# Kernel tuning notes

Measured on AMD Instinct MI355X. Metric: run time of the kernel, lower is better.

The kernel has to match this reference:

```python
import jax, jax.numpy as jnp
import numpy as np

B, R, NT = 1, 384, 4        # batch, num_res, num_templates
C_IN = 128                   # rep_2d num_c (pair channels)
C_KV = 64                    # template pair channels
H, C = 4, 64                 # num_heads, attention_num_c


def setup_inputs() -> dict:
    key = jax.random.key(0)
    ks = jax.random.split(key, 7)
    s = lambda fan_in: 1.0 / np.sqrt(fan_in)
    return {
        "z2d": jax.random.normal(ks[0], (B, R, R, C_IN), jnp.float32),
        "t2d": jax.random.normal(ks[1], (B, NT, R, R, C_KV), jnp.float32),
        # weights stored [in, out] (torch nn.Linear applies x @ W.T)
        "Wq": jax.random.normal(ks[2], (C_IN, H * C), jnp.float32) * s(C_IN),
        "Wk": jax.random.normal(ks[3], (C_KV, H * C), jnp.float32) * s(C_KV),
        "Wv": jax.random.normal(ks[4], (C_KV, H * C), jnp.float32) * s(C_KV),
        "Wo": jax.random.normal(ks[5], (H * C, C_IN), jnp.float32) * s(H * C),
        "bo": jax.random.normal(ks[6], (C_IN,), jnp.float32) * s(H * C),
    }


def reference(z2d, t2d, Wq, Wk, Wv, Wo, bo):
    b, r, _, c_in = z2d.shape
    nt = t2d.shape[1]
    P = r * r  # flattened residue-pair axis

    z = z2d.reshape(b, P, 1, c_in)                             # [b, P, 1, c_in]
    t = jnp.transpose(t2d, (0, 2, 3, 1, 4)).reshape(b, P, nt, -1)  # [b, P, K, c_kv]

    q = (z @ Wq).reshape(b, P, 1, H, C) * C ** (-0.5)          # [b, P, 1, h, c]
    k = (t @ Wk).reshape(b, P, nt, H, C)                       # [b, P, k, h, c]
    v = (t @ Wv).reshape(b, P, nt, H, C)

    logits = jnp.einsum('bpqhc,bpkhc->bphqk', q, k)            # softmax over k templates
    weights = jax.nn.softmax(logits, axis=-1)
    weighted_avg = jnp.einsum('bphqk,bpkhc->bpqhc', weights, v)  # [b, P, 1, h, c]

    out = weighted_avg.reshape(b, P, 1, H * C) @ Wo + bo
    return out.reshape(b, r, r, c_in)
```

## Files before the change

kernel.cpp:

```cpp
#include <hip/hip_runtime.h>
#include <hip/hip_bf16.h>

#define R_   384
#define P_   (R_ * R_)
#define NT_  4
#define CIN  128
#define CKV  64
#define NH   4
#define HC   256

#define TP   64
#define LDZ  136
#define LDA  280

typedef __attribute__((ext_vector_type(8))) short bf16x8;
typedef __attribute__((ext_vector_type(4))) float f32x4;
typedef __attribute__((ext_vector_type(4))) uint  u32x4;
typedef __attribute__((ext_vector_type(2))) __bf16 bfv2;

#if defined(__has_builtin)
#if __has_builtin(__builtin_amdgcn_fdot2_f32_bf16)
#define HAS_DOT2BF 1
#endif
#endif

__device__ __forceinline__ ushort f2bf_s(float f) {
    uint32_t u = __float_as_uint(f);
    u += 0x7FFFu + ((u >> 16) & 1u);
    return (ushort)(u >> 16);
}
__device__ __forceinline__ uint packbf2(float lo, float hi) {
    return (uint)f2bf_s(lo) | ((uint)f2bf_s(hi) << 16);
}
__device__ __forceinline__ uint2 pack4(const float4 v) {
    uint2 r; r.x = packbf2(v.x, v.y); r.y = packbf2(v.z, v.w); return r;
}
__device__ __forceinline__ float bflo(uint t) { return __uint_as_float(t << 16); }
__device__ __forceinline__ float bfhi(uint t) { return __uint_as_float(t & 0xffff0000u); }

__device__ __forceinline__ float dot2bf(uint a, uint b, float acc) {
#ifdef HAS_DOT2BF
    union { uint u; bfv2 v; } ua, ub;
    ua.u = a; ub.u = b;
    return __builtin_amdgcn_fdot2_f32_bf16(ua.v, ub.v, acc, false);
#else
    float r = fmaf(bflo(a), bflo(b), acc);
    return fmaf(bfhi(a), bfhi(b), r);
#endif
}

__global__ __launch_bounds__(256) void precompute_mg(
        const float* __restrict__ Wq, const float* __restrict__ Wk,
        const float* __restrict__ Wv, const float* __restrict__ Wo,
        ushort* __restrict__ Mt, ushort* __restrict__ Gt) {
    int tid = blockIdx.x * blockDim.x + threadIdx.x;
    if (tid < HC * CIN) {
        int n = tid >> 7, ci = tid & 127;
        int h = n >> 6, j = n & 63;
        float acc = 0.f;
        for (int c = 0; c < 64; ++c)
            acc += Wq[ci * HC + h * 64 + c] * Wk[j * HC + h * 64 + c];
        Mt[n * CIN + ci] = f2bf_s(acc * 0.125f);
    } else {
        int t = tid - HC * CIN;
        int co = t >> 8, n = t & 255;
        int h = n >> 6, j = n & 63;
        float acc = 0.f;
        for (int c = 0; c < 64; ++c)
            acc += Wv[j * HC + h * 64 + c] * Wo[(h * 64 + c) * CIN + co];
        Gt[co * HC + n] = f2bf_s(acc);
    }
}

__global__ __launch_bounds__(256, 2) void tpa_fused(
        const float* __restrict__ z2d, const float* __restrict__ t2d,
        const ushort* __restrict__ Mt, const ushort* __restrict__ Gt,
        const float* __restrict__ bo, float* __restrict__ out) {

    __shared__ ushort s0[TP * LDA];
    __shared__ ushort sT[TP * LDA];

    const int tid  = threadIdx.x;
    const int lane = tid & 63;
    const int wv   = tid >> 6;
    const int lr   = lane & 15;
    const int lk   = (lane >> 4) << 3;
    const int pg0  = blockIdx.x * TP;

    bf16x8 B1[4][4];
    #pragma unroll
    for (int kt = 0; kt < 4; ++kt)
        #pragma unroll
        for (int nt = 0; nt < 4; ++nt)
            B1[kt][nt] = *(const bf16x8*)(Mt + (wv * 64 + nt * 16 + lr) * CIN + kt * 32 + lk);
    bf16x8 B2[8][2];
    #pragma unroll
    for (int kt = 0; kt < 8; ++kt)
        #pragma unroll
        for (int nt = 0; nt < 2; ++nt)
            B2[kt][nt] = *(const bf16x8*)(Gt + (wv * 32 + nt * 16 + lr) * HC + kt * 32 + lk);

    const float bias0 = bo[wv * 32 + lr];
    const float bias1 = bo[wv * 32 + 16 + lr];

    #pragma unroll
    for (int i = 0; i < 8; ++i) {
        int idx = (i * 256 + tid) * 4, p = idx >> 7, c = idx & 127;
        float4 v = *(const float4*)(z2d + (size_t)(pg0 + p) * CIN + c);
        *(uint2*)&s0[p * LDZ + c] = pack4(v);
    }
    #pragma unroll
    for (int k = 0; k < NT_; ++k) {
        const float* src = t2d + ((size_t)k * P_ + pg0) * CKV;
        #pragma unroll
        for (int i = 0; i < 4; ++i) {
            int idx = (i * 256 + tid) * 4, p = idx >> 6, c = idx & 63;
            float4 v = *(const float4*)(src + p * 64 + c);
            *(uint2*)&sT[p * LDA + k * 64 + c] = pack4(v);
        }
    }
    __syncthreads();

    f32x4 acc1[4][4];
    #pragma unroll
    for (int mt = 0; mt < 4; ++mt)
        #pragma unroll
        for (int nt = 0; nt < 4; ++nt)
            acc1[mt][nt] = (f32x4){0.f, 0.f, 0.f, 0.f};
    #pragma unroll
    for (int kt = 0; kt < 4; ++kt) {
        bf16x8 af[4];
        #pragma unroll
        for (int mt = 0; mt < 4; ++mt)
            af[mt] = *(const bf16x8*)&s0[(mt * 16 + lr) * LDZ + kt * 32 + lk];
        #pragma unroll
        for (int mt = 0; mt < 4; ++mt)
            #pragma unroll
            for (int nt = 0; nt < 4; ++nt)
                acc1[mt][nt] = __builtin_amdgcn_mfma_f32_16x16x32_bf16(
                    af[mt], B1[kt][nt], acc1[mt][nt], 0, 0, 0);
    }
    __syncthreads();

    #pragma unroll
    for (int mt = 0; mt < 4; ++mt) {
        int row = mt * 16 + ((lane >> 4) << 2);
        #pragma unroll
        for (int nt = 0; nt < 4; ++nt) {
            int n = wv * 64 + nt * 16 + lr;
            #pragma unroll
            for (int r = 0; r < 4; ++r)
                s0[(row + r) * LDA + n] = f2bf_s(acc1[mt][nt][r]);
        }
    }
    asm volatile("s_waitcnt lgkmcnt(0)" ::: "memory");
    __builtin_amdgcn_sched_barrier(0);

    {
        ushort* arow = &s0[lane * LDA + wv * 64];
        const ushort* trow = &sT[lane * LDA];

        u32x4 a4[8];
        #pragma unroll
        for (int q = 0; q < 8; ++q) a4[q] = *(const u32x4*)&arow[q * 8];

        float lg[4];
        #pragma unroll
        for (int k = 0; k < 4; ++k) {
            float s = 0.f;
            #pragma unroll
            for (int q = 0; q < 8; ++q) {
                u32x4 tq = *(const u32x4*)&trow[k * 64 + q * 8];
                #pragma unroll
                for (int e = 0; e < 4; ++e)
                    s = dot2bf(a4[q][e], tq[e], s);
            }
            lg[k] = s;
        }
        float mx = fmaxf(fmaxf(lg[0], lg[1]), fmaxf(lg[2], lg[3]));
        float w0 = __expf(lg[0] - mx), w1 = __expf(lg[1] - mx);
        float w2 = __expf(lg[2] - mx), w3 = __expf(lg[3] - mx);
        float inv = 1.f / (w0 + w1 + w2 + w3);
        w0 *= inv; w1 *= inv; w2 *= inv; w3 *= inv;

        #pragma unroll
        for (int q = 0; q < 8; ++q) {
            u32x4 t0 = *(const u32x4*)&trow[q * 8];
            u32x4 t1 = *(const u32x4*)&trow[64 + q * 8];
            u32x4 t2 = *(const u32x4*)&trow[128 + q * 8];
            u32x4 t3 = *(const u32x4*)&trow[192 + q * 8];
            u32x4 o;
            #pragma unroll
            for (int e = 0; e < 4; ++e) {
                float lo = w0 * bflo(t0[e]) + w1 * bflo(t1[e]) + w2 * bflo(t2[e]) + w3 * bflo(t3[e]);
                float hi = w0 * bfhi(t0[e]) + w1 * bfhi(t1[e]) + w2 * bfhi(t2[e]) + w3 * bfhi(t3[e]);
                o[e] = packbf2(lo, hi);
            }
            *(u32x4*)&arow[q * 8] = o;
        }
    }
    __syncthreads();

    f32x4 acc2[4][2];
    #pragma unroll
    for (int mt = 0; mt < 4; ++mt)
        #pragma unroll
        for (int nt = 0; nt < 2; ++nt)
            acc2[mt][nt] = (f32x4){0.f, 0.f, 0.f, 0.f};
    #pragma unroll
    for (int kt = 0; kt < 8; ++kt) {
        bf16x8 af[4];
        #pragma unroll
        for (int mt = 0; mt < 4; ++mt)
            af[mt] = *(const bf16x8*)&s0[(mt * 16 + lr) * LDA + kt * 32 + lk];
        #pragma unroll
        for (int mt = 0; mt < 4; ++mt)
            #pragma unroll
            for (int nt = 0; nt < 2; ++nt)
                acc2[mt][nt] = __builtin_amdgcn_mfma_f32_16x16x32_bf16(
                    af[mt], B2[kt][nt], acc2[mt][nt], 0, 0, 0);
    }

    #pragma unroll
    for (int nt = 0; nt < 2; ++nt) {
        int co = wv * 32 + nt * 16 + lr;
        float bias = nt ? bias1 : bias0;
        #pragma unroll
        for (int mt = 0; mt < 4; ++mt) {
            int row = mt * 16 + ((lane >> 4) << 2);
            #pragma unroll
            for (int r = 0; r < 4; ++r)
                out[(size_t)(pg0 + row + r) * CIN + co] = acc2[mt][nt][r] + bias;
        }
    }
}

extern "C" void kernel_launch(void* const* d_in, const int* in_sizes, int n_in,
                              void* d_out, int out_size, void* d_ws, size_t ws_size,
                              hipStream_t stream) {
    const float* z2d = (const float*)d_in[0];
    const float* t2d = (const float*)d_in[1];
    const float* Wq  = (const float*)d_in[2];
    const float* Wk  = (const float*)d_in[3];
    const float* Wv  = (const float*)d_in[4];
    const float* Wo  = (const float*)d_in[5];
    const float* bo  = (const float*)d_in[6];

    ushort* Mt = (ushort*)d_ws;
    ushort* Gt = Mt + HC * CIN;

    precompute_mg<<<(2 * HC * CIN) / 256, 256, 0, stream>>>(Wq, Wk, Wv, Wo, Mt, Gt);
    tpa_fused<<<P_ / TP, 256, 0, stream>>>(z2d, t2d, Mt, Gt, bo, (float*)d_out);
}
```

Baseline: 82.40 us.

## Stream z and templates directly from global, drop template LDS staging, swap MFMA operands

The z tile is now loaded straight from global memory into MFMA fragments instead of being staged through LDS. Template rows are read directly from global in fp32 for both the logit and weighted-sum passes. This removes the sT buffer and halves shared memory, and the occupancy hint rises from 2 to 3 blocks. MFMA operands are swapped so outputs come out transposed, which allows packed 8-byte LDS writes and float4 global stores. In exchange each thread reads every template row from global twice, and the logits now use fp32 template values rather than bf16.

```diff
diff --git a/kernel.cpp b/kernel.cpp
--- a/kernel.cpp
+++ b/kernel.cpp
@@ -1,5 +1,4 @@
 #include <hip/hip_runtime.h>
-#include <hip/hip_bf16.h>
 
 #define R_   384
 #define P_   (R_ * R_)
@@ -10,19 +9,11 @@
 #define HC   256
 
 #define TP   64
-#define LDZ  136
 #define LDA  280
 
 typedef __attribute__((ext_vector_type(8))) short bf16x8;
 typedef __attribute__((ext_vector_type(4))) float f32x4;
 typedef __attribute__((ext_vector_type(4))) uint  u32x4;
-typedef __attribute__((ext_vector_type(2))) __bf16 bfv2;
-
-#if defined(__has_builtin)
-#if __has_builtin(__builtin_amdgcn_fdot2_f32_bf16)
-#define HAS_DOT2BF 1
-#endif
-#endif
 
 __device__ __forceinline__ ushort f2bf_s(float f) {
     uint32_t u = __float_as_uint(f);
@@ -32,22 +23,10 @@
 __device__ __forceinline__ uint packbf2(float lo, float hi) {
     return (uint)f2bf_s(lo) | ((uint)f2bf_s(hi) << 16);
 }
-__device__ __forceinline__ uint2 pack4(const float4 v) {
-    uint2 r; r.x = packbf2(v.x, v.y); r.y = packbf2(v.z, v.w); return r;
-}
 __device__ __forceinline__ float bflo(uint t) { return __uint_as_float(t << 16); }
 __device__ __forceinline__ float bfhi(uint t) { return __uint_as_float(t & 0xffff0000u); }
 
-__device__ __forceinline__ float dot2bf(uint a, uint b, float acc) {
-#ifdef HAS_DOT2BF
-    union { uint u; bfv2 v; } ua, ub;
-    ua.u = a; ub.u = b;
-    return __builtin_amdgcn_fdot2_f32_bf16(ua.v, ub.v, acc, false);
-#else
-    float r = fmaf(bflo(a), bflo(b), acc);
-    return fmaf(bfhi(a), bfhi(b), r);
-#endif
-}
+union BF8 { bf16x8 v; uint u[4]; };
 
 __global__ __launch_bounds__(256) void precompute_mg(
         const float* __restrict__ Wq, const float* __restrict__ Wk,
@@ -72,19 +51,19 @@
     }
 }
 
-__global__ __launch_bounds__(256, 2) void tpa_fused(
+__global__ __launch_bounds__(256, 3) void tpa_fused(
         const float* __restrict__ z2d, const float* __restrict__ t2d,
         const ushort* __restrict__ Mt, const ushort* __restrict__ Gt,
         const float* __restrict__ bo, float* __restrict__ out) {
 
-    __shared__ ushort s0[TP * LDA];
-    __shared__ ushort sT[TP * LDA];
+    __shared__ ushort sA[TP * LDA];
 
     const int tid  = threadIdx.x;
     const int lane = tid & 63;
     const int wv   = tid >> 6;
     const int lr   = lane & 15;
-    const int lk   = (lane >> 4) << 3;
+    const int g    = lane >> 4;
+    const int g8   = g << 3;
     const int pg0  = blockIdx.x * TP;
 
     bf16x8 B1[4][4];
@@ -92,145 +71,157 @@
     for (int kt = 0; kt < 4; ++kt)
         #pragma unroll
         for (int nt = 0; nt < 4; ++nt)
-            B1[kt][nt] = *(const bf16x8*)(Mt + (wv * 64 + nt * 16 + lr) * CIN + kt * 32 + lk);
+            B1[kt][nt] = *(const bf16x8*)(Mt + (wv * 64 + nt * 16 + lr) * CIN + kt * 32 + g8);
+
+    f32x4 acc1[4][4];
+    #pragma unroll
+    for (int nt = 0; nt < 4; ++nt)
+        #pragma unroll
+        for (int mt = 0; mt < 4; ++mt)
+            acc1[nt][mt] = (f32x4){0.f, 0.f, 0.f, 0.f};
+
+    #pragma unroll
+    for (int kt = 0; kt < 4; ++kt) {
+        bf16x8 zf[4];
+        #pragma unroll
+        for (int mt = 0; mt < 4; ++mt) {
+            const float* zp = z2d + (size_t)(pg0 + mt * 16 + lr) * CIN + kt * 32 + g8;
+            float4 z0 = *(const float4*)zp;
+            float4 z1 = *(const float4*)(zp + 4);
+            BF8 zb;
+            zb.u[0] = packbf2(z0.x, z0.y); zb.u[1] = packbf2(z0.z, z0.w);
+            zb.u[2] = packbf2(z1.x, z1.y); zb.u[3] = packbf2(z1.z, z1.w);
+            zf[mt] = zb.v;
+        }
+        #pragma unroll
+        for (int nt = 0; nt < 4; ++nt)
+            #pragma unroll
+            for (int mt = 0; mt < 4; ++mt)
+                acc1[nt][mt] = __builtin_amdgcn_mfma_f32_16x16x32_bf16(
+                    B1[kt][nt], zf[mt], acc1[nt][mt], 0, 0, 0);
+    }
+
+    #pragma unroll
+    for (int nt = 0; nt < 4; ++nt) {
+        int n0 = wv * 64 + nt * 16 + g * 4;
+        #pragma unroll
+        for (int mt = 0; mt < 4; ++mt) {
+            int p = mt * 16 + lr;
+            uint2 w;
+            w.x = packbf2(acc1[nt][mt][0], acc1[nt][mt][1]);
+            w.y = packbf2(acc1[nt][mt][2], acc1[nt][mt][3]);
+            *(uint2*)&sA[p * LDA + n0] = w;
+        }
+    }
+
     bf16x8 B2[8][2];
     #pragma unroll
     for (int kt = 0; kt < 8; ++kt)
         #pragma unroll
         for (int nt = 0; nt < 2; ++nt)
-            B2[kt][nt] = *(const bf16x8*)(Gt + (wv * 32 + nt * 16 + lr) * HC + kt * 32 + lk);
-
-    const float bias0 = bo[wv * 32 + lr];
-    const float bias1 = bo[wv * 32 + 16 + lr];
-
-    #pragma unroll
-    for (int i = 0; i < 8; ++i) {
-        int idx = (i * 256 + tid) * 4, p = idx >> 7, c = idx & 127;
-        float4 v = *(const float4*)(z2d + (size_t)(pg0 + p) * CIN + c);
-        *(uint2*)&s0[p * LDZ + c] = pack4(v);
-    }
-    #pragma unroll
-    for (int k = 0; k < NT_; ++k) {
-        const float* src = t2d + ((size_t)k * P_ + pg0) * CKV;
-        #pragma unroll
-        for (int i = 0; i < 4; ++i) {
-            int idx = (i * 256 + tid) * 4, p = idx >> 6, c = idx & 63;
-            float4 v = *(const float4*)(src + p * 64 + c);
-            *(uint2*)&sT[p * LDA + k * 64 + c] = pack4(v);
-        }
-    }
+            B2[kt][nt] = *(const bf16x8*)(Gt + (wv * 32 + nt * 16 + lr) * HC + kt * 32 + g8);
+    float4 b4[2];
+    #pragma unroll
+    for (int nt = 0; nt < 2; ++nt)
+        b4[nt] = *(const float4*)(bo + wv * 32 + nt * 16 + g * 4);
+
     __syncthreads();
 
-    f32x4 acc1[4][4];
-    #pragma unroll
-    for (int mt = 0; mt < 4; ++mt)
-        #pragma unroll
-        for (int nt = 0; nt < 4; ++nt)
-            acc1[mt][nt] = (f32x4){0.f, 0.f, 0.f, 0.f};
-    #pragma unroll
-    for (int kt = 0; kt < 4; ++kt) {
-        bf16x8 af[4];
-        #pragma unroll
-        for (int mt = 0; mt < 4; ++mt)
-            af[mt] = *(const bf16x8*)&s0[(mt * 16 + lr) * LDZ + kt * 32 + lk];
-        #pragma unroll
-        for (int mt = 0; mt < 4; ++mt)
-            #pragma unroll
-            for (int nt = 0; nt < 4; ++nt)
-                acc1[mt][nt] = __builtin_amdgcn_mfma_f32_16x16x32_bf16(
-                    af[mt], B1[kt][nt], acc1[mt][nt], 0, 0, 0);
-    }
-    __syncthreads();
-
-    #pragma unroll
-    for (int mt = 0; mt < 4; ++mt) {
-        int row = mt * 16 + ((lane >> 4) << 2);
-        #pragma unroll
-        for (int nt = 0; nt < 4; ++nt) {
-            int n = wv * 64 + nt * 16 + lr;
-            #pragma unroll
-            for (int r = 0; r < 4; ++r)
-                s0[(row + r) * LDA + n] = f2bf_s(acc1[mt][nt][r]);
-        }
-    }
-    asm volatile("s_waitcnt lgkmcnt(0)" ::: "memory");
-    __builtin_amdgcn_sched_barrier(0);
-
     {
-        ushort* arow = &s0[lane * LDA + wv * 64];
-        const ushort* trow = &sT[lane * LDA];
+        const int h = g;
+        const int p = wv * 16 + lr;
+        const ushort* arow = &sA[p * LDA + h * 64];
 
         u32x4 a4[8];
         #pragma unroll
         for (int q = 0; q < 8; ++q) a4[q] = *(const u32x4*)&arow[q * 8];
 
-        float lg[4];
-        #pragma unroll
-        for (int k = 0; k < 4; ++k) {
-            float s = 0.f;
-            #pragma unroll
-            for (int q = 0; q < 8; ++q) {
-                u32x4 tq = *(const u32x4*)&trow[k * 64 + q * 8];
-                #pragma unroll
-                for (int e = 0; e < 4; ++e)
-                    s = dot2bf(a4[q][e], tq[e], s);
-            }
-            lg[k] = s;
-        }
-        float mx = fmaxf(fmaxf(lg[0], lg[1]), fmaxf(lg[2], lg[3]));
-        float w0 = __expf(lg[0] - mx), w1 = __expf(lg[1] - mx);
-        float w2 = __expf(lg[2] - mx), w3 = __expf(lg[3] - mx);
+        const float* tk0 = t2d + ((size_t)0 * P_ + pg0 + p) * CKV;
+        const float* tk1 = t2d + ((size_t)1 * P_ + pg0 + p) * CKV;
+        const float* tk2 = t2d + ((size_t)2 * P_ + pg0 + p) * CKV;
+        const float* tk3 = t2d + ((size_t)3 * P_ + pg0 + p) * CKV;
+
+        float lg0 = 0.f, lg1 = 0.f, lg2 = 0.f, lg3 = 0.f;
+        #pragma unroll
+        for (int q4 = 0; q4 < 16; ++q4) {
+            float4 t0 = *(const float4*)(tk0 + q4 * 4);
+            float4 t1 = *(const float4*)(tk1 + q4 * 4);
+            float4 t2 = *(const float4*)(tk2 + q4 * 4);
+            float4 t3 = *(const float4*)(tk3 + q4 * 4);
+            uint ua = a4[q4 >> 1][(q4 & 1) * 2 + 0];
+            uint ub = a4[q4 >> 1][(q4 & 1) * 2 + 1];
+            float a0 = bflo(ua), a1 = bfhi(ua), a2 = bflo(ub), a3 = bfhi(ub);
+            lg0 = fmaf(a0, t0.x, lg0); lg0 = fmaf(a1, t0.y, lg0);
+            lg0 = fmaf(a2, t0.z, lg0); lg0 = fmaf(a3, t0.w, lg0);
+            lg1 = fmaf(a0, t1.x, lg1); lg1 = fmaf(a1, t1.y, lg1);
+            lg1 = fmaf(a2, t1.z, lg1); lg1 = fmaf(a3, t1.w, lg1);
+            lg2 = fmaf(a0, t2.x, lg2); lg2 = fmaf(a1, t2.y, lg2);
+            lg2 = fmaf(a2, t2.z, lg2); lg2 = fmaf(a3, t2.w, lg2);
+            lg3 = fmaf(a0, t3.x, lg3); lg3 = fmaf(a1, t3.y, lg3);
+            lg3 = fmaf(a2, t3.z, lg3); lg3 = fmaf(a3, t3.w, lg3);
+        }
+        float mx = fmaxf(fmaxf(lg0, lg1), fmaxf(lg2, lg3));
+        float w0 = __expf(lg0 - mx), w1 = __expf(lg1 - mx);
+        float w2 = __expf(lg2 - mx), w3 = __expf(lg3 - mx);
         float inv = 1.f / (w0 + w1 + w2 + w3);
         w0 *= inv; w1 *= inv; w2 *= inv; w3 *= inv;
 
-        #pragma unroll
-        for (int q = 0; q < 8; ++q) {
-            u32x4 t0 = *(const u32x4*)&trow[q * 8];
-            u32x4 t1 = *(const u32x4*)&trow[64 + q * 8];
-            u32x4 t2 = *(const u32x4*)&trow[128 + q * 8];
-            u32x4 t3 = *(const u32x4*)&trow[192 + q * 8];
+        ushort* urow = &sA[p * LDA + h * 64];
+        #pragma unroll
+        for (int q8 = 0; q8 < 8; ++q8) {
+            float4 t0a = *(const float4*)(tk0 + q8 * 8), t0b = *(const float4*)(tk0 + q8 * 8 + 4);
+            float4 t1a = *(const float4*)(tk1 + q8 * 8), t1b = *(const float4*)(tk1 + q8 * 8 + 4);
+            float4 t2a = *(const float4*)(tk2 + q8 * 8), t2b = *(const float4*)(tk2 + q8 * 8 + 4);
+            float4 t3a = *(const float4*)(tk3 + q8 * 8), t3b = *(const float4*)(tk3 + q8 * 8 + 4);
+            float u0 = w0*t0a.x + w1*t1a.x + w2*t2a.x + w3*t3a.x;
+            float u1 = w0*t0a.y + w1*t1a.y + w2*t2a.y + w3*t3a.y;
+            float u2 = w0*t0a.z + w1*t1a.z + w2*t2a.z + w3*t3a.z;
+            float u3 = w0*t0a.w + w1*t1a.w + w2*t2a.w + w3*t3a.w;
+            float u4 = w0*t0b.x + w1*t1b.x + w2*t2b.x + w3*t3b.x;
+            float u5 = w0*t0b.y + w1*t1b.y + w2*t2b.y + w3*t3b.y;
+            float u6 = w0*t0b.z + w1*t1b.z + w2*t2b.z + w3*t3b.z;
+            float u7 = w0*t0b.w + w1*t1b.w + w2*t2b.w + w3*t3b.w;
             u32x4 o;
+            o[0] = packbf2(u0, u1); o[1] = packbf2(u2, u3);
+            o[2] = packbf2(u4, u5); o[3] = packbf2(u6, u7);
+            *(u32x4*)&urow[q8 * 8] = o;
+        }
+    }
+    __syncthreads();
+
+    f32x4 acc2[2][4];
+    #pragma unroll
+    for (int nt = 0; nt < 2; ++nt)
+        #pragma unroll
+        for (int mt = 0; mt < 4; ++mt)
+            acc2[nt][mt] = (f32x4){0.f, 0.f, 0.f, 0.f};
+
+    #pragma unroll
+    for (int kt = 0; kt < 8; ++kt) {
+        bf16x8 uf[4];
+        #pragma unroll
+        for (int mt = 0; mt < 4; ++mt)
+            uf[mt] = *(const bf16x8*)&sA[(mt * 16 + lr) * LDA + kt * 32 + g8];
+        #pragma unroll
+        for (int nt = 0; nt < 2; ++nt)
             #pragma unroll
-            for (int e = 0; e < 4; ++e) {
-                float lo = w0 * bflo(t0[e]) + w1 * bflo(t1[e]) + w2 * bflo(t2[e]) + w3 * bflo(t3[e]);
-                float hi = w0 * bfhi(t0[e]) + w1 * bfhi(t1[e]) + w2 * bfhi(t2[e]) + w3 * bfhi(t3[e]);
-                o[e] = packbf2(lo, hi);
-            }
-            *(u32x4*)&arow[q * 8] = o;
-        }
-    }
-    __syncthreads();
-
-    f32x4 acc2[4][2];
-    #pragma unroll
-    for (int mt = 0; mt < 4; ++mt)
-        #pragma unroll
-        for (int nt = 0; nt < 2; ++nt)
-            acc2[mt][nt] = (f32x4){0.f, 0.f, 0.f, 0.f};
-    #pragma unroll
-    for (int kt = 0; kt < 8; ++kt) {
-        bf16x8 af[4];
-        #pragma unroll
-        for (int mt = 0; mt < 4; ++mt)
-            af[mt] = *(const bf16x8*)&s0[(mt * 16 + lr) * LDA + kt * 32 + lk];
-        #pragma unroll
-        for (int mt = 0; mt < 4; ++mt)
-            #pragma unroll
-            for (int nt = 0; nt < 2; ++nt)
-                acc2[mt][nt] = __builtin_amdgcn_mfma_f32_16x16x32_bf16(
-                    af[mt], B2[kt][nt], acc2[mt][nt], 0, 0, 0);
+            for (int mt = 0; mt < 4; ++mt)
+                acc2[nt][mt] = __builtin_amdgcn_mfma_f32_16x16x32_bf16(
+                    B2[kt][nt], uf[mt], acc2[nt][mt], 0, 0, 0);
     }
 
     #pragma unroll
     for (int nt = 0; nt < 2; ++nt) {
-        int co = wv * 32 + nt * 16 + lr;
-        float bias = nt ? bias1 : bias0;
+        int co0 = wv * 32 + nt * 16 + g * 4;
         #pragma unroll
         for (int mt = 0; mt < 4; ++mt) {
-            int row = mt * 16 + ((lane >> 4) << 2);
-            #pragma unroll
-            for (int r = 0; r < 4; ++r)
-                out[(size_t)(pg0 + row + r) * CIN + co] = acc2[mt][nt][r] + bias;
+            int p = mt * 16 + lr;
+            float4 o;
+            o.x = acc2[nt][mt][0] + b4[nt].x;
+            o.y = acc2[nt][mt][1] + b4[nt].y;
+            o.z = acc2[nt][mt][2] + b4[nt].z;
+            o.w = acc2[nt][mt][3] + b4[nt].w;
+            *(float4*)(out + (size_t)(pg0 + p) * CIN + co0) = o;
         }
     }
 }
```

After: 282.7 us. 3.43x slower.

## Split fused template attention across 8 waves per block

Applied to the files above, without the earlier changes.

The block doubles from 4 to 8 waves, and the work is repartitioned. GEMM1 is split by head and row half. The softmax stage uses two lanes per pair, with a shuffle to combine the partial logits. GEMM2 gives each wave 16 output columns. Global loads are issued into registers before the LDS stores, and the B2 weight load is deferred until after the softmax stage. The aim is to cut register pressure and raise occupancy so more memory latency is hidden. The cost is extra shuffles and a per-lane reload of the weight fragments.

```diff
diff --git a/kernel.cpp b/kernel.cpp
--- a/kernel.cpp
+++ b/kernel.cpp
@@ -1,5 +1,4 @@
 #include <hip/hip_runtime.h>
-#include <hip/hip_bf16.h>
 
 #define R_   384
 #define P_   (R_ * R_)
@@ -72,7 +71,7 @@
     }
 }
 
-__global__ __launch_bounds__(256, 2) void tpa_fused(
+__global__ __launch_bounds__(512, 4) void tpa_fused(
         const float* __restrict__ z2d, const float* __restrict__ t2d,
         const ushort* __restrict__ Mt, const ushort* __restrict__ Gt,
         const float* __restrict__ bo, float* __restrict__ out) {
@@ -82,59 +81,66 @@
 
     const int tid  = threadIdx.x;
     const int lane = tid & 63;
-    const int wv   = tid >> 6;
+    const int w    = tid >> 6;
+    const int h    = w >> 1;
+    const int ph   = w & 1;
     const int lr   = lane & 15;
-    const int lk   = (lane >> 4) << 3;
+    const int g    = lane >> 4;
+    const int lk   = g << 3;
     const int pg0  = blockIdx.x * TP;
 
-    bf16x8 B1[4][4];
-    #pragma unroll
-    for (int kt = 0; kt < 4; ++kt)
-        #pragma unroll
-        for (int nt = 0; nt < 4; ++nt)
-            B1[kt][nt] = *(const bf16x8*)(Mt + (wv * 64 + nt * 16 + lr) * CIN + kt * 32 + lk);
-    bf16x8 B2[8][2];
-    #pragma unroll
-    for (int kt = 0; kt < 8; ++kt)
-        #pragma unroll
-        for (int nt = 0; nt < 2; ++nt)
-            B2[kt][nt] = *(const bf16x8*)(Gt + (wv * 32 + nt * 16 + lr) * HC + kt * 32 + lk);
-
-    const float bias0 = bo[wv * 32 + lr];
-    const float bias1 = bo[wv * 32 + 16 + lr];
-
-    #pragma unroll
-    for (int i = 0; i < 8; ++i) {
-        int idx = (i * 256 + tid) * 4, p = idx >> 7, c = idx & 127;
-        float4 v = *(const float4*)(z2d + (size_t)(pg0 + p) * CIN + c);
-        *(uint2*)&s0[p * LDZ + c] = pack4(v);
-    }
+    float4 zv[4];
+    #pragma unroll
+    for (int i = 0; i < 4; ++i) {
+        int idx = (i * 512 + tid) * 4, p = idx >> 7, c = idx & 127;
+        zv[i] = *(const float4*)(z2d + (size_t)(pg0 + p) * CIN + c);
+    }
+    float4 tv[8];
     #pragma unroll
     for (int k = 0; k < NT_; ++k) {
         const float* src = t2d + ((size_t)k * P_ + pg0) * CKV;
         #pragma unroll
-        for (int i = 0; i < 4; ++i) {
-            int idx = (i * 256 + tid) * 4, p = idx >> 6, c = idx & 63;
-            float4 v = *(const float4*)(src + p * 64 + c);
-            *(uint2*)&sT[p * LDA + k * 64 + c] = pack4(v);
-        }
-    }
+        for (int i = 0; i < 2; ++i) {
+            int idx = (i * 512 + tid) * 4, p = idx >> 6, c = idx & 63;
+            tv[k * 2 + i] = *(const float4*)(src + p * 64 + c);
+        }
+    }
+    #pragma unroll
+    for (int i = 0; i < 4; ++i) {
+        int idx = (i * 512 + tid) * 4, p = idx >> 7, c = idx & 127;
+        *(uint2*)&s0[p * LDZ + c] = pack4(zv[i]);
+    }
+    #pragma unroll
+    for (int k = 0; k < NT_; ++k)
+        #pragma unroll
+        for (int i = 0; i < 2; ++i) {
+            int idx = (i * 512 + tid) * 4, p = idx >> 6, c = idx & 63;
+            *(uint2*)&sT[p * LDA + k * 64 + c] = pack4(tv[k * 2 + i]);
+        }
+
+    bf16x8 B1[4][4];
+    #pragma unroll
+    for (int kt = 0; kt < 4; ++kt)
+        #pragma unroll
+        for (int nt = 0; nt < 4; ++nt)
+            B1[kt][nt] = *(const bf16x8*)(Mt + (h * 64 + nt * 16 + lr) * CIN + kt * 32 + lk);
+
     __syncthreads();
 
-    f32x4 acc1[4][4];
-    #pragma unroll
-    for (int mt = 0; mt < 4; ++mt)
+    f32x4 acc1[2][4];
+    #pragma unroll
+    for (int mt = 0; mt < 2; ++mt)
         #pragma unroll
         for (int nt = 0; nt < 4; ++nt)
             acc1[mt][nt] = (f32x4){0.f, 0.f, 0.f, 0.f};
     #pragma unroll
     for (int kt = 0; kt < 4; ++kt) {
-        bf16x8 af[4];
-        #pragma unroll
-        for (int mt = 0; mt < 4; ++mt)
-            af[mt] = *(const bf16x8*)&s0[(mt * 16 + lr) * LDZ + kt * 32 + lk];
-        #pragma unroll
-        for (int mt = 0; mt < 4; ++mt)
+        bf16x8 af[2];
+        #pragma unroll
+        for (int mt = 0; mt < 2; ++mt)
+            af[mt] = *(const bf16x8*)&s0[(ph * 32 + mt * 16 + lr) * LDZ + kt * 32 + lk];
+        #pragma unroll
+        for (int mt = 0; mt < 2; ++mt)
             #pragma unroll
             for (int nt = 0; nt < 4; ++nt)
                 acc1[mt][nt] = __builtin_amdgcn_mfma_f32_16x16x32_bf16(
@@ -143,11 +149,11 @@
     __syncthreads();
 
     #pragma unroll
-    for (int mt = 0; mt < 4; ++mt) {
-        int row = mt * 16 + ((lane >> 4) << 2);
+    for (int mt = 0; mt < 2; ++mt) {
+        int row = ph * 32 + mt * 16 + g * 4;
         #pragma unroll
         for (int nt = 0; nt < 4; ++nt) {
-            int n = wv * 64 + nt * 16 + lr;
+            int n = h * 64 + nt * 16 + lr;
             #pragma unroll
             for (int r = 0; r < 4; ++r)
                 s0[(row + r) * LDA + n] = f2bf_s(acc1[mt][nt][r]);
@@ -157,24 +163,27 @@
     __builtin_amdgcn_sched_barrier(0);
 
     {
-        ushort* arow = &s0[lane * LDA + wv * 64];
-        const ushort* trow = &sT[lane * LDA];
-
-        u32x4 a4[8];
-        #pragma unroll
-        for (int q = 0; q < 8; ++q) a4[q] = *(const u32x4*)&arow[q * 8];
+        const int p  = ph * 32 + (lane & 31);
+        const int ch = (lane >> 5) << 5;
+        ushort* arow = &s0[p * LDA + h * 64 + ch];
+        const ushort* trow = &sT[p * LDA + ch];
+
+        u32x4 a4[4];
+        #pragma unroll
+        for (int q = 0; q < 4; ++q) a4[q] = *(const u32x4*)&arow[q * 8];
 
         float lg[4];
         #pragma unroll
         for (int k = 0; k < 4; ++k) {
             float s = 0.f;
             #pragma unroll
-            for (int q = 0; q < 8; ++q) {
+            for (int q = 0; q < 4; ++q) {
                 u32x4 tq = *(const u32x4*)&trow[k * 64 + q * 8];
                 #pragma unroll
                 for (int e = 0; e < 4; ++e)
                     s = dot2bf(a4[q][e], tq[e], s);
             }
+            s += __shfl_xor(s, 32);
             lg[k] = s;
         }
         float mx = fmaxf(fmaxf(lg[0], lg[1]), fmaxf(lg[2], lg[3]));
@@ -184,7 +193,7 @@
         w0 *= inv; w1 *= inv; w2 *= inv; w3 *= inv;
 
         #pragma unroll
-        for (int q = 0; q < 8; ++q) {
+        for (int q = 0; q < 4; ++q) {
             u32x4 t0 = *(const u32x4*)&trow[q * 8];
             u32x4 t1 = *(const u32x4*)&trow[64 + q * 8];
             u32x4 t2 = *(const u32x4*)&trow[128 + q * 8];
@@ -201,12 +210,16 @@
     }
     __syncthreads();
 
-    f32x4 acc2[4][2];
+    bf16x8 B2[8];
+    #pragma unroll
+    for (int kt = 0; kt < 8; ++kt)
+        B2[kt] = *(const bf16x8*)(Gt + (w * 16 + lr) * HC + kt * 32 + lk);
+    const float bias = bo[w * 16 + lr];
+
+    f32x4 acc2[4];
     #pragma unroll
     for (int mt = 0; mt < 4; ++mt)
-        #pragma unroll
-        for (int nt = 0; nt < 2; ++nt)
-            acc2[mt][nt] = (f32x4){0.f, 0.f, 0.f, 0.f};
+        acc2[mt] = (f32x4){0.f, 0.f, 0.f, 0.f};
     #pragma unroll
     for (int kt = 0; kt < 8; ++kt) {
         bf16x8 af[4];
@@ -215,23 +228,16 @@
             af[mt] = *(const bf16x8*)&s0[(mt * 16 + lr) * LDA + kt * 32 + lk];
         #pragma unroll
         for (int mt = 0; mt < 4; ++mt)
-            #pragma unroll
-            for (int nt = 0; nt < 2; ++nt)
-                acc2[mt][nt] = __builtin_amdgcn_mfma_f32_16x16x32_bf16(
-                    af[mt], B2[kt][nt], acc2[mt][nt], 0, 0, 0);
-    }
-
-    #pragma unroll
-    for (int nt = 0; nt < 2; ++nt) {
-        int co = wv * 32 + nt * 16 + lr;
-        float bias = nt ? bias1 : bias0;
-        #pragma unroll
-        for (int mt = 0; mt < 4; ++mt) {
-            int row = mt * 16 + ((lane >> 4) << 2);
-            #pragma unroll
-            for (int r = 0; r < 4; ++r)
-                out[(size_t)(pg0 + row + r) * CIN + co] = acc2[mt][nt][r] + bias;
-        }
+            acc2[mt] = __builtin_amdgcn_mfma_f32_16x16x32_bf16(
+                af[mt], B2[kt], acc2[mt], 0, 0, 0);
+    }
+
+    #pragma unroll
+    for (int mt = 0; mt < 4; ++mt) {
+        int row = mt * 16 + g * 4;
+        #pragma unroll
+        for (int r = 0; r < 4; ++r)
+            out[(size_t)(pg0 + row + r) * CIN + w * 16 + lr] = acc2[mt][r] + bias;
     }
 }
 
@@ -250,5 +256,5 @@
     ushort* Gt = Mt + HC * CIN;
 
     precompute_mg<<<(2 * HC * CIN) / 256, 256, 0, stream>>>(Wq, Wk, Wv, Wo, Mt, Gt);
-    tpa_fused<<<P_ / TP, 256, 0, stream>>>(z2d, t2d, Mt, Gt, bo, (float*)d_out);
-}
+    tpa_fused<<<P_ / TP, 512, 0, stream>>>(z2d, t2d, Mt, Gt, bo, (float*)d_out);
+}
```

Result: slower. 104.1 us (median of 4 runs) (+26.4%).

## Keep template tiles in registers, shrink LDS, and raise occupancy to three blocks

Applied to the files above, without the earlier changes.

Template data for the block's 64 pairs now goes straight from global memory into registers, packed as bf16, so the separate shared-memory tile for it is gone. Each thread holds a 16-channel slice per template, and partial logits are combined with cross-lane shuffles. The first GEMM swaps its operands so packed bf16 pairs can be written to LDS as 8-byte stores. Weight fragments are loaded per half of the K loop, and B2 is loaded only after the first GEMM, to cut register pressure so launch bounds can allow three blocks per CU. The cost is extra shuffle work and possible register spills.

```diff
diff --git a/kernel.cpp b/kernel.cpp
--- a/kernel.cpp
+++ b/kernel.cpp
@@ -1,5 +1,4 @@
 #include <hip/hip_runtime.h>
-#include <hip/hip_bf16.h>
 
 #define R_   384
 #define P_   (R_ * R_)
@@ -72,131 +71,157 @@
     }
 }
 
-__global__ __launch_bounds__(256, 2) void tpa_fused(
+__global__ __launch_bounds__(256, 3) void tpa_fused(
         const float* __restrict__ z2d, const float* __restrict__ t2d,
         const ushort* __restrict__ Mt, const ushort* __restrict__ Gt,
         const float* __restrict__ bo, float* __restrict__ out) {
 
-    __shared__ ushort s0[TP * LDA];
-    __shared__ ushort sT[TP * LDA];
+    __shared__ ushort s0z[TP * LDZ];
+    __shared__ ushort s0a[TP * LDA];
 
     const int tid  = threadIdx.x;
     const int lane = tid & 63;
     const int wv   = tid >> 6;
     const int lr   = lane & 15;
-    const int lk   = (lane >> 4) << 3;
+    const int g    = lane >> 4;
+    const int g8   = g << 3;
     const int pg0  = blockIdx.x * TP;
-
-    bf16x8 B1[4][4];
-    #pragma unroll
-    for (int kt = 0; kt < 4; ++kt)
-        #pragma unroll
-        for (int nt = 0; nt < 4; ++nt)
-            B1[kt][nt] = *(const bf16x8*)(Mt + (wv * 64 + nt * 16 + lr) * CIN + kt * 32 + lk);
-    bf16x8 B2[8][2];
-    #pragma unroll
-    for (int kt = 0; kt < 8; ++kt)
-        #pragma unroll
-        for (int nt = 0; nt < 2; ++nt)
-            B2[kt][nt] = *(const bf16x8*)(Gt + (wv * 32 + nt * 16 + lr) * HC + kt * 32 + lk);
-
-    const float bias0 = bo[wv * 32 + lr];
-    const float bias1 = bo[wv * 32 + 16 + lr];
+    const int pm   = wv * 16 + lr;
+
+    u32x4 tb[NT_][2];
+    #pragma unroll
+    for (int k = 0; k < NT_; ++k) {
+        const float* tp = t2d + ((size_t)k * P_ + pg0 + pm) * CKV + g * 16;
+        float4 ta = *(const float4*)(tp);
+        float4 tb4 = *(const float4*)(tp + 4);
+        float4 tc = *(const float4*)(tp + 8);
+        float4 td = *(const float4*)(tp + 12);
+        tb[k][0][0] = packbf2(ta.x, ta.y); tb[k][0][1] = packbf2(ta.z, ta.w);
+        tb[k][0][2] = packbf2(tb4.x, tb4.y); tb[k][0][3] = packbf2(tb4.z, tb4.w);
+        tb[k][1][0] = packbf2(tc.x, tc.y); tb[k][1][1] = packbf2(tc.z, tc.w);
+        tb[k][1][2] = packbf2(td.x, td.y); tb[k][1][3] = packbf2(td.z, td.w);
+    }
 
     #pragma unroll
     for (int i = 0; i < 8; ++i) {
         int idx = (i * 256 + tid) * 4, p = idx >> 7, c = idx & 127;
         float4 v = *(const float4*)(z2d + (size_t)(pg0 + p) * CIN + c);
-        *(uint2*)&s0[p * LDZ + c] = pack4(v);
-    }
-    #pragma unroll
-    for (int k = 0; k < NT_; ++k) {
-        const float* src = t2d + ((size_t)k * P_ + pg0) * CKV;
-        #pragma unroll
-        for (int i = 0; i < 4; ++i) {
-            int idx = (i * 256 + tid) * 4, p = idx >> 6, c = idx & 63;
-            float4 v = *(const float4*)(src + p * 64 + c);
-            *(uint2*)&sT[p * LDA + k * 64 + c] = pack4(v);
-        }
+        *(uint2*)&s0z[p * LDZ + c] = pack4(v);
     }
     __syncthreads();
 
     f32x4 acc1[4][4];
     #pragma unroll
-    for (int mt = 0; mt < 4; ++mt)
-        #pragma unroll
-        for (int nt = 0; nt < 4; ++nt)
-            acc1[mt][nt] = (f32x4){0.f, 0.f, 0.f, 0.f};
-    #pragma unroll
-    for (int kt = 0; kt < 4; ++kt) {
-        bf16x8 af[4];
+    for (int nt = 0; nt < 4; ++nt)
         #pragma unroll
         for (int mt = 0; mt < 4; ++mt)
-            af[mt] = *(const bf16x8*)&s0[(mt * 16 + lr) * LDZ + kt * 32 + lk];
-        #pragma unroll
-        for (int mt = 0; mt < 4; ++mt)
+            acc1[nt][mt] = (f32x4){0.f, 0.f, 0.f, 0.f};
+
+    #pragma unroll
+    for (int half = 0; half < 2; ++half) {
+        bf16x8 B1[2][4];
+        #pragma unroll
+        for (int kt2 = 0; kt2 < 2; ++kt2)
             #pragma unroll
             for (int nt = 0; nt < 4; ++nt)
-                acc1[mt][nt] = __builtin_amdgcn_mfma_f32_16x16x32_bf16(
-                    af[mt], B1[kt][nt], acc1[mt][nt], 0, 0, 0);
+                B1[kt2][nt] = *(const bf16x8*)(Mt + (wv * 64 + nt * 16 + lr) * CIN
+                                               + (half * 2 + kt2) * 32 + g8);
+        #pragma unroll
+        for (int kt2 = 0; kt2 < 2; ++kt2) {
+            int kt = half * 2 + kt2;
+            bf16x8 zf[4];
+            #pragma unroll
+            for (int mt = 0; mt < 4; ++mt)
+                zf[mt] = *(const bf16x8*)&s0z[(mt * 16 + lr) * LDZ + kt * 32 + g8];
+            #pragma unroll
+            for (int nt = 0; nt < 4; ++nt)
+                #pragma unroll
+                for (int mt = 0; mt < 4; ++mt)
+                    acc1[nt][mt] = __builtin_amdgcn_mfma_f32_16x16x32_bf16(
+                        B1[kt2][nt], zf[mt], acc1[nt][mt], 0, 0, 0);
+        }
+    }
+
+    #pragma unroll
+    for (int nt = 0; nt < 4; ++nt) {
+        int n0 = wv * 64 + nt * 16 + g * 4;
+        #pragma unroll
+        for (int mt = 0; mt < 4; ++mt) {
+            int p = mt * 16 + lr;
+            uint2 w;
+            w.x = packbf2(acc1[nt][mt][0], acc1[nt][mt][1]);
+            w.y = packbf2(acc1[nt][mt][2], acc1[nt][mt][3]);
+            *(uint2*)&s0a[p * LDA + n0] = w;
+        }
     }
     __syncthreads();
 
-    #pragma unroll
-    for (int mt = 0; mt < 4; ++mt) {
-        int row = mt * 16 + ((lane >> 4) << 2);
-        #pragma unroll
-        for (int nt = 0; nt < 4; ++nt) {
-            int n = wv * 64 + nt * 16 + lr;
-            #pragma unroll
-            for (int r = 0; r < 4; ++r)
-                s0[(row + r) * LDA + n] = f2bf_s(acc1[mt][nt][r]);
-        }
-    }
-    asm volatile("s_waitcnt lgkmcnt(0)" ::: "memory");
-    __builtin_amdgcn_sched_barrier(0);
+    bf16x8 B2[8][2];
+    #pragma unroll
+    for (int kt = 0; kt < 8; ++kt)
+        #pragma unroll
+        for (int nt = 0; nt < 2; ++nt)
+            B2[kt][nt] = *(const bf16x8*)(Gt + (wv * 32 + nt * 16 + lr) * HC + kt * 32 + g8);
+    const float bias0 = bo[wv * 32 + lr];
+    const float bias1 = bo[wv * 32 + 16 + lr];
 
     {
-        ushort* arow = &s0[lane * LDA + wv * 64];
-        const ushort* trow = &sT[lane * LDA];
-
-        u32x4 a4[8];
-        #pragma unroll
-        for (int q = 0; q < 8; ++q) a4[q] = *(const u32x4*)&arow[q * 8];
-
-        float lg[4];
-        #pragma unroll
-        for (int k = 0; k < 4; ++k) {
-            float s = 0.f;
-            #pragma unroll
-            for (int q = 0; q < 8; ++q) {
-                u32x4 tq = *(const u32x4*)&trow[k * 64 + q * 8];
+        u32x4 a2[4][2];
+        #pragma unroll
+        for (int h = 0; h < 4; ++h) {
+            a2[h][0] = *(const u32x4*)&s0a[pm * LDA + h * 64 + g * 16];
+            a2[h][1] = *(const u32x4*)&s0a[pm * LDA + h * 64 + g * 16 + 8];
+        }
+
+        float lg[4][4];
+        #pragma unroll
+        for (int h = 0; h < 4; ++h)
+            #pragma unroll
+            for (int k = 0; k < NT_; ++k) {
+                float s = 0.f;
                 #pragma unroll
-                for (int e = 0; e < 4; ++e)
-                    s = dot2bf(a4[q][e], tq[e], s);
+                for (int j = 0; j < 2; ++j)
+                    #pragma unroll
+                    for (int e = 0; e < 4; ++e)
+                        s = dot2bf(a2[h][j][e], tb[k][j][e], s);
+                lg[h][k] = s;
             }
-            lg[k] = s;
-        }
-        float mx = fmaxf(fmaxf(lg[0], lg[1]), fmaxf(lg[2], lg[3]));
-        float w0 = __expf(lg[0] - mx), w1 = __expf(lg[1] - mx);
-        float w2 = __expf(lg[2] - mx), w3 = __expf(lg[3] - mx);
-        float inv = 1.f / (w0 + w1 + w2 + w3);
-        w0 *= inv; w1 *= inv; w2 *= inv; w3 *= inv;
-
-        #pragma unroll
-        for (int q = 0; q < 8; ++q) {
-            u32x4 t0 = *(const u32x4*)&trow[q * 8];
-            u32x4 t1 = *(const u32x4*)&trow[64 + q * 8];
-            u32x4 t2 = *(const u32x4*)&trow[128 + q * 8];
-            u32x4 t3 = *(const u32x4*)&trow[192 + q * 8];
-            u32x4 o;
-            #pragma unroll
-            for (int e = 0; e < 4; ++e) {
-                float lo = w0 * bflo(t0[e]) + w1 * bflo(t1[e]) + w2 * bflo(t2[e]) + w3 * bflo(t3[e]);
-                float hi = w0 * bfhi(t0[e]) + w1 * bfhi(t1[e]) + w2 * bfhi(t2[e]) + w3 * bfhi(t3[e]);
-                o[e] = packbf2(lo, hi);
+        #pragma unroll
+        for (int h = 0; h < 4; ++h)
+            #pragma unroll
+            for (int k = 0; k < NT_; ++k) {
+                float s = lg[h][k];
+                s += __shfl_xor(s, 16);
+                s += __shfl_xor(s, 32);
+                lg[h][k] = s;
             }
-            *(u32x4*)&arow[q * 8] = o;
+        float wgt[4][4];
+        #pragma unroll
+        for (int h = 0; h < 4; ++h) {
+            float mx = fmaxf(fmaxf(lg[h][0], lg[h][1]), fmaxf(lg[h][2], lg[h][3]));
+            float e0 = __expf(lg[h][0] - mx), e1 = __expf(lg[h][1] - mx);
+            float e2 = __expf(lg[h][2] - mx), e3 = __expf(lg[h][3] - mx);
+            float inv = 1.f / (e0 + e1 + e2 + e3);
+            wgt[h][0] = e0 * inv; wgt[h][1] = e1 * inv;
+            wgt[h][2] = e2 * inv; wgt[h][3] = e3 * inv;
+        }
+        #pragma unroll
+        for (int h = 0; h < 4; ++h) {
+            #pragma unroll
+            for (int j = 0; j < 2; ++j) {
+                u32x4 o;
+                #pragma unroll
+                for (int e = 0; e < 4; ++e) {
+                    uint t0 = tb[0][j][e], t1 = tb[1][j][e];
+                    uint t2 = tb[2][j][e], t3 = tb[3][j][e];
+                    float lo = wgt[h][0] * bflo(t0) + wgt[h][1] * bflo(t1)
+                             + wgt[h][2] * bflo(t2) + wgt[h][3] * bflo(t3);
+                    float hi = wgt[h][0] * bfhi(t0) + wgt[h][1] * bfhi(t1)
+                             + wgt[h][2] * bfhi(t2) + wgt[h][3] * bfhi(t3);
+                    o[e] = packbf2(lo, hi);
+                }
+                *(u32x4*)&s0a[pm * LDA + h * 64 + g * 16 + j * 8] = o;
+            }
         }
     }
     __syncthreads();
@@ -212,7 +237,7 @@
         bf16x8 af[4];
         #pragma unroll
         for (int mt = 0; mt < 4; ++mt)
-            af[mt] = *(const bf16x8*)&s0[(mt * 16 + lr) * LDA + kt * 32 + lk];
+            af[mt] = *(const bf16x8*)&s0a[(mt * 16 + lr) * LDA + kt * 32 + g8];
         #pragma unroll
         for (int mt = 0; mt < 4; ++mt)
             #pragma unroll
@@ -227,7 +252,7 @@
         float bias = nt ? bias1 : bias0;
         #pragma unroll
         for (int mt = 0; mt < 4; ++mt) {
-            int row = mt * 16 + ((lane >> 4) << 2);
+            int row = mt * 16 + g * 4;
             #pragma unroll
             for (int r = 0; r < 4; ++r)
                 out[(size_t)(pg0 + row + r) * CIN + co] = acc2[mt][nt][r] + bias;
```

Result: slower. 115.7 us (+40.4%).
